# Optimization experiments

Hardware: AMD Instinct MI355X
Metric: run time of the kernel (lower is better)

Reference implementation:

```python
import jax, jax.numpy as jnp
import numpy as np
from jax import lax

NEG = -1e30  # finite stand-in for -inf so logaddexp grads stay finite


def setup_inputs() -> dict:
    key = jax.random.key(0)
    k1, k2, k3, k4, k5 = jax.random.split(key, 5)
    B, T, L, S = 16, 2048, 256, 8
    return {
        "emissions": jax.random.normal(k1, (B, T, S), dtype=jnp.float32),
        "transition": jax.random.normal(k2, (S, S), dtype=jnp.float32),
        "bos": jax.random.normal(k3, (S,), dtype=jnp.float32),
        "eos": jax.random.normal(k4, (S,), dtype=jnp.float32),
        "lengths": jnp.full((B,), T, dtype=jnp.int32),
        "targets": jax.random.randint(k5, (B, L), 0, 4, dtype=jnp.int32),
        "target_lengths": jnp.full((B,), L, dtype=jnp.int32),
    }


def _den_logz(em, lengths, transition, bos, eos):
    # Exact log-semiring forward over the fully-connected 8-state denominator CRF graph
    # (the limit of k2.intersect_dense_pruned(...).get_tot_scores(log_semiring=True)).
    B, T, S = em.shape
    alpha0 = bos[None, :] + em[:, 0, :]  # (B,S)

    def step(alpha, em_t):
        a = jax.nn.logsumexp(alpha[:, :, None] + transition[None, :, :], axis=1) + em_t
        return a, a

    _, alphas = lax.scan(step, alpha0, jnp.swapaxes(em, 0, 1)[1:])  # (T-1,B,S)
    alphas = jnp.concatenate([alpha0[None], alphas], axis=0)  # (T,B,S)
    fin = alphas[lengths - 1, jnp.arange(B)]  # (B,S) alpha at last valid frame
    return jax.nn.logsumexp(fin + eos[None, :], axis=-1)


def _num_logz(em, lengths, targets, target_lengths, transition, bos, eos):
    # Forward over the target-constrained enter/extend lattice: symbol u must be
    # entered (state targets[u]) exactly once, optionally extended (state targets[u]+4),
    # then the path moves monotonically to symbol u+1.
    B, T, S = em.shape
    L = targets.shape[1]
    b_idx = jnp.arange(B)
    es = targets          # enter-state ids, (B,L)
    xs = targets + 4      # extend-state ids, (B,L)

    t_xx = transition[xs, xs]  # extend_u -> extend_u
    t_ex = transition[es, xs]  # enter_u  -> extend_u
    prev_e = jnp.concatenate([es[:, :1], es[:, :-1]], axis=1)
    prev_x = jnp.concatenate([xs[:, :1], xs[:, :-1]], axis=1)
    t_ee = transition[prev_e, es]  # enter_{u-1}  -> enter_u
    t_xe = transition[prev_x, es]  # extend_{u-1} -> enter_u

    a_e0 = jnp.full((B, L), NEG, dtype=em.dtype)
    a_e0 = a_e0.at[:, 0].set(bos[es[:, 0]] + em[b_idx, 0, es[:, 0]])
    a_x0 = jnp.full((B, L), NEG, dtype=em.dtype)

    def shift(a):  # a[:, u-1], NEG at u=0
        return jnp.concatenate([jnp.full((B, 1), NEG, dtype=a.dtype), a[:, :-1]], axis=1)

    def step(carry, em_t):
        a_e, a_x = carry
        em_e = jnp.take_along_axis(em_t, es, axis=1)  # (B,L)
        em_x = jnp.take_along_axis(em_t, xs, axis=1)
        new_e = em_e + jnp.logaddexp(shift(a_e) + t_ee, shift(a_x) + t_xe)
        new_x = em_x + jnp.logaddexp(a_e + t_ex, a_x + t_xx)
        return (new_e, new_x), (new_e, new_x)

    _, (ae, ax) = lax.scan(step, (a_e0, a_x0), jnp.swapaxes(em, 0, 1)[1:])
    ae = jnp.concatenate([a_e0[None], ae], axis=0)  # (T,B,L)
    ax = jnp.concatenate([a_x0[None], ax], axis=0)
    fin_e = ae[lengths - 1, b_idx]  # (B,L)
    fin_x = ax[lengths - 1, b_idx]
    u = target_lengths - 1
    fe = fin_e[b_idx, u] + eos[es[b_idx, u]]
    fx = fin_x[b_idx, u] + eos[xs[b_idx, u]]
    return jnp.logaddexp(fe, fx)  # (B,)


def reference(emissions, transition, bos, eos, lengths, targets, target_lengths):
    em = emissions.astype(jnp.float32)
    logz_den = _den_logz(em, lengths, transition, bos, eos)
    logz_num = _num_logz(em, lengths, targets, target_lengths, transition, bos, eos)
    # all samples valid by construction (lengths > 0, 0 < target_len <= length)
    return jnp.mean(logz_den - logz_num)
```

## Files before the change

kernel.cpp:

```cpp
#include <hip/hip_runtime.h>
#include <math.h>


#define LOG2E 1.4426950408889634f
#define LN2   0.69314718055994531f
#define CTL_WSHL1  0x130
#define CTL_WSHR1  0x138
#define CTL_ROR(r) (0x120 + (r))

template <int CTRL>
__device__ __forceinline__ float fdpp(float x) {
    return __int_as_float(__builtin_amdgcn_update_dpp(
        0, __float_as_int(x), CTRL, 0xF, 0xF, true));
}
template <int CTRL>
__device__ __forceinline__ int idpp(int x) {
    return __builtin_amdgcn_update_dpp(0, x, CTRL, 0xF, 0xF, true);
}
__device__ __forceinline__ void cfence() { asm volatile("" ::: "memory"); }

__device__ __forceinline__ float fexp2(float x) {
#if __has_builtin(__builtin_amdgcn_exp2f)
    return __builtin_amdgcn_exp2f(x);
#else
    return exp2f(x);
#endif
}
__device__ __forceinline__ float flog2(float x) {
#if __has_builtin(__builtin_amdgcn_logf)
    return __builtin_amdgcn_logf(x);
#else
    return __log2f(x);
#endif
}
__device__ __forceinline__ float lse2(float a, float b) {
    float m = fmaxf(a, b);
    float d = fminf(a, b) - m;
    return m + flog2(1.0f + fexp2(d));
}

struct NumC { float tee[4], txe[4], tex[4], txx[4]; };

__device__ __forceinline__ void numf_step(const float2* p, float* E, float* X,
                                          float teeF, float txeF, const NumC& c) {
    float nbE = fdpp<CTL_WSHR1>(E[3]);
    float nbX = fdpp<CTL_WSHR1>(X[3]);
    float nE0 = p[0].x * fmaf(nbE,  teeF,     nbX  * txeF);
    float nE1 = p[1].x * fmaf(E[0], c.tee[1], X[0] * c.txe[1]);
    float nE2 = p[2].x * fmaf(E[1], c.tee[2], X[1] * c.txe[2]);
    float nE3 = p[3].x * fmaf(E[2], c.tee[3], X[2] * c.txe[3]);
    float nX0 = p[0].y * fmaf(E[0], c.tex[0], X[0] * c.txx[0]);
    float nX1 = p[1].y * fmaf(E[1], c.tex[1], X[1] * c.txx[1]);
    float nX2 = p[2].y * fmaf(E[2], c.tex[2], X[2] * c.txx[2]);
    float nX3 = p[3].y * fmaf(E[3], c.tex[3], X[3] * c.txx[3]);
    E[0] = nE0; E[1] = nE1; E[2] = nE2; E[3] = nE3;
    X[0] = nX0; X[1] = nX1; X[2] = nX2; X[3] = nX3;
}

__device__ __forceinline__ void numf_boundary(float* E, float* X, int& s,
                                              float& teeF, float& txeF,
                                              int lane, const NumC& c) {
    float m = fmaxf(fmaxf(fmaxf(E[0], E[1]), fmaxf(E[2], E[3])),
                    fmaxf(fmaxf(X[0], X[1]), fmaxf(X[2], X[3])));
    const bool live = (m > 0.0f);
    const int ex = live ? ((int)(__float_as_uint(m) >> 23) - 126) : 0;
    s += ex;
    const int bs = idpp<CTL_WSHR1>(s);
    if (!live) s = bs;
    int d = (lane == 0) ? 0 : (bs - s);
    const int extra = (d > 30) ? d : 0;
    s += extra; d -= extra;
    const float fsc = ldexpf(1.0f, -(ex + extra));
#pragma unroll
    for (int k = 0; k < 4; ++k) { E[k] *= fsc; X[k] *= fsc; }
    const float fs0 = (lane == 0) ? 0.0f : ldexpf(1.0f, d);
    teeF = c.tee[0] * fs0;
    txeF = c.txe[0] * fs0;
}

__device__ __forceinline__ void numb_step(const float2* p, float* bE, float* bX,
                                          const float* tex, const float* txx,
                                          const float* teeN, const float* txeN,
                                          float teeN3F, float txeN3F) {
    float mm0 = p[0].x * bE[0];
    float mm1 = p[1].x * bE[1];
    float mm2 = p[2].x * bE[2];
    float mm3 = p[3].x * bE[3];
    float m10 = p[0].y * bX[0];
    float m11 = p[1].y * bX[1];
    float m12 = p[2].y * bX[2];
    float m13 = p[3].y * bX[3];
    float mup = fdpp<CTL_WSHL1>(mm0);
    float nE0 = fmaf(tex[0], m10, teeN[0] * mm1);
    float nE1 = fmaf(tex[1], m11, teeN[1] * mm2);
    float nE2 = fmaf(tex[2], m12, teeN[2] * mm3);
    float nE3 = fmaf(tex[3], m13, teeN3F   * mup);
    float nX0 = fmaf(txx[0], m10, txeN[0] * mm1);
    float nX1 = fmaf(txx[1], m11, txeN[1] * mm2);
    float nX2 = fmaf(txx[2], m12, txeN[2] * mm3);
    float nX3 = fmaf(txx[3], m13, txeN3F   * mup);
    bE[0] = nE0; bE[1] = nE1; bE[2] = nE2; bE[3] = nE3;
    bX[0] = nX0; bX[1] = nX1; bX[2] = nX2; bX[3] = nX3;
}

__device__ __forceinline__ void numb_boundary(float* bE, float* bX, int& s,
                                              float& teeN3F, float& txeN3F,
                                              int lane, float teeN3, float txeN3) {
    float m = fmaxf(fmaxf(fmaxf(bE[0], bE[1]), fmaxf(bE[2], bE[3])),
                    fmaxf(fmaxf(bX[0], bX[1]), fmaxf(bX[2], bX[3])));
    const bool live = (m > 0.0f);
    const int ex = live ? ((int)(__float_as_uint(m) >> 23) - 126) : 0;
    s += ex;
    const int bs = idpp<CTL_WSHL1>(s);
    if (!live) s = bs;
    int d = (lane == 63) ? 0 : (bs - s);
    const int extra = (d > 30) ? d : 0;
    s += extra; d -= extra;
    const float fsc = ldexpf(1.0f, -(ex + extra));
#pragma unroll
    for (int k = 0; k < 4; ++k) { bE[k] *= fsc; bX[k] *= fsc; }
    const float fs = (lane == 63) ? 0.0f : ldexpf(1.0f, d);
    teeN3F = teeN3 * fs;
    txeN3F = txeN3 * fs;
}

__device__ __forceinline__ float denf_step(float al, float emt, const float* Tr) {
    float v1 = fdpp<CTL_ROR(1)>(al);
    float v2 = fdpp<CTL_ROR(2)>(al);
    float v3 = fdpp<CTL_ROR(3)>(al);
    float v4 = fdpp<CTL_ROR(4)>(al);
    float v5 = fdpp<CTL_ROR(5)>(al);
    float v6 = fdpp<CTL_ROR(6)>(al);
    float v7 = fdpp<CTL_ROR(7)>(al);
    float q0 = fmaf(v1, Tr[1], al * Tr[0]);
    float q1 = fmaf(v3, Tr[3], v2 * Tr[2]);
    float q2 = fmaf(v5, Tr[5], v4 * Tr[4]);
    float q3 = fmaf(v7, Tr[7], v6 * Tr[6]);
    return ((q0 + q1) + (q2 + q3)) * emt;
}
__device__ __forceinline__ float denb_step(float al, float emt, const float* TrB) {
    float g  = al * emt;
    float v1 = fdpp<CTL_ROR(7)>(g);
    float v2 = fdpp<CTL_ROR(6)>(g);
    float v3 = fdpp<CTL_ROR(5)>(g);
    float v4 = fdpp<CTL_ROR(4)>(g);
    float v5 = fdpp<CTL_ROR(3)>(g);
    float v6 = fdpp<CTL_ROR(2)>(g);
    float v7 = fdpp<CTL_ROR(1)>(g);
    float q0 = fmaf(v1, TrB[1], g * TrB[0]);
    float q1 = fmaf(v3, TrB[3], v2 * TrB[2]);
    float q2 = fmaf(v5, TrB[5], v4 * TrB[4]);
    float q3 = fmaf(v7, TrB[7], v6 * TrB[6]);
    return (q0 + q1) + (q2 + q3);
}

extern "C" __global__ void __launch_bounds__(256)
crf_fused(const float* __restrict__ em, const float* __restrict__ trans,
          const float* __restrict__ bos, const float* __restrict__ eos,
          const int* __restrict__ lengths, const int* __restrict__ targets,
          const int* __restrict__ tlens,
          float* __restrict__ ws, float* __restrict__ out,
          int B, int T, int S, int L)
{
    extern __shared__ float sm[];
    const int b    = blockIdx.x;
    const int tid  = threadIdx.x;
    const int half = S >> 1;
    const float* gem = em + (size_t)b * T * S;
    const int len = lengths[b];
    const int tm  = (len - 1) >> 1;

    float* numF  = sm + T * 8;
    float* numB  = numF + 512;
    int*   numFs = (int*)(numB + 512);
    int*   numBs = numFs + 64;
    float* denF  = (float*)(numBs + 64);
    float* denB  = denF + 8;
    int*   denFs = (int*)(denB + 8);
    int*   denBs = denFs + 8;

    for (int t = tid; t < T; t += 256) {
        const float4* gr = (const float4*)(gem + t * S);
        float4 a = gr[0], c4 = gr[1];
        float4 w0, w1;
        w0.x = fexp2(a.x * LOG2E); w0.y = fexp2(c4.x * LOG2E);
        w0.z = fexp2(a.y * LOG2E); w0.w = fexp2(c4.y * LOG2E);
        w1.x = fexp2(a.z * LOG2E); w1.y = fexp2(c4.z * LOG2E);
        w1.z = fexp2(a.w * LOG2E); w1.w = fexp2(c4.w * LOG2E);
        ((float4*)sm)[t * 2]     = w0;
        ((float4*)sm)[t * 2 + 1] = w1;
    }
    __syncthreads();

    const int wv   = tid >> 6;
    const int lane = tid & 63;
    const float2* sm2 = (const float2*)sm;

    if (wv == 0) {
        const int u0 = lane * 4;
        int e[4], ep[4];
        const int base = b * L;
#pragma unroll
        for (int k = 0; k < 4; ++k) {
            int u = u0 + k;
            e[k] = targets[base + ((u < L) ? u : (L - 1))];
        }
        ep[0] = (u0 > 0) ? targets[base + u0 - 1] : e[0];
        ep[1] = e[0]; ep[2] = e[1]; ep[3] = e[2];
        NumC c;
#pragma unroll
        for (int k = 0; k < 4; ++k) {
            c.tee[k] = fexp2(trans[ep[k] * S + e[k]] * LOG2E);
            c.txe[k] = fexp2(trans[(ep[k] + half) * S + e[k]] * LOG2E);
            c.tex[k] = fexp2(trans[e[k] * S + e[k] + half] * LOG2E);
            c.txx[k] = fexp2(trans[(e[k] + half) * S + e[k] + half] * LOG2E);
        }
        float E[4] = {0.f,0.f,0.f,0.f}, X[4] = {0.f,0.f,0.f,0.f};
        int s = 0;
        if (lane == 0) E[0] = fexp2(bos[e[0]] * LOG2E) * sm2[e[0]].x;
        float teeF = (lane == 0) ? 0.0f : c.tee[0];
        float txeF = (lane == 0) ? 0.0f : c.txe[0];

        float2 A[4][4], Bf[4][4];
        int t0 = 1;
#pragma unroll
        for (int q = 0; q < 4; ++q) {
            int tq = t0 + q; if (tq > tm) tq = (tm > 0) ? tm : 0;
#pragma unroll
            for (int k = 0; k < 4; ++k) A[q][k] = sm2[tq * 4 + e[k]];
        }
        cfence();
        while (t0 + 7 <= tm) {
#pragma unroll
            for (int q = 0; q < 4; ++q)
#pragma unroll
                for (int k = 0; k < 4; ++k)
                    Bf[q][k] = sm2[(t0 + 4 + q) * 4 + e[k]];
            cfence();
#pragma unroll
            for (int q = 0; q < 4; ++q) numf_step(A[q], E, X, teeF, txeF, c);
#pragma unroll
            for (int q = 0; q < 4; ++q) {
                int tq = t0 + 8 + q; if (tq > tm) tq = tm;
#pragma unroll
                for (int k = 0; k < 4; ++k) A[q][k] = sm2[tq * 4 + e[k]];
            }
            cfence();
#pragma unroll
            for (int q = 0; q < 4; ++q) numf_step(Bf[q], E, X, teeF, txeF, c);
            numf_boundary(E, X, s, teeF, txeF, lane, c);
            t0 += 8;
        }
        while (t0 <= tm) {
            float2 p[4];
#pragma unroll
            for (int k = 0; k < 4; ++k) p[k] = sm2[t0 * 4 + e[k]];
            numf_step(p, E, X, teeF, txeF, c);
            ++t0;
        }
#pragma unroll
        for (int k = 0; k < 4; ++k) {
            numF[lane * 8 + k]     = E[k];
            numF[lane * 8 + 4 + k] = X[k];
        }
        numFs[lane] = s;
    } else if (wv == 1) {
        const int u0 = lane * 4;
        int e[5];
        const int base = b * L;
#pragma unroll
        for (int k = 0; k < 5; ++k) {
            int u = u0 + k;
            e[k] = targets[base + ((u < L) ? u : (L - 1))];
        }
        float tex[4], txx[4], teeN[4], txeN[4];
#pragma unroll
        for (int k = 0; k < 4; ++k) {
            tex[k]  = fexp2(trans[e[k] * S + e[k] + half] * LOG2E);
            txx[k]  = fexp2(trans[(e[k] + half) * S + e[k] + half] * LOG2E);
            teeN[k] = fexp2(trans[e[k] * S + e[k + 1]] * LOG2E);
            txeN[k] = fexp2(trans[(e[k] + half) * S + e[k + 1]] * LOG2E);
        }
        if (lane == 63) { teeN[3] = 0.0f; txeN[3] = 0.0f; }
        float bE[4] = {0.f,0.f,0.f,0.f}, bX[4] = {0.f,0.f,0.f,0.f};
        const int uf = tlens[b] - 1;
        if (lane == (uf >> 2)) {
            const int kf = uf & 3;
            const int ef = e[kf];
            bE[kf] = fexp2(eos[ef] * LOG2E);
            bX[kf] = fexp2(eos[ef + half] * LOG2E);
        }
        int s = 0;
        float teeN3F = teeN[3], txeN3F = txeN[3];

        float2 A[4][4], Bf[4][4];
        int t1 = len - 1;
        const int tlo = tm + 1;
#pragma unroll
        for (int q = 0; q < 4; ++q) {
            int tq = t1 - q; if (tq < tlo) tq = tlo;
#pragma unroll
            for (int k = 0; k < 4; ++k) A[q][k] = sm2[tq * 4 + e[k]];
        }
        cfence();
        while (t1 - 7 >= tlo) {
#pragma unroll
            for (int q = 0; q < 4; ++q)
#pragma unroll
                for (int k = 0; k < 4; ++k)
                    Bf[q][k] = sm2[(t1 - 4 - q) * 4 + e[k]];
            cfence();
#pragma unroll
            for (int q = 0; q < 4; ++q)
                numb_step(A[q], bE, bX, tex, txx, teeN, txeN, teeN3F, txeN3F);
#pragma unroll
            for (int q = 0; q < 4; ++q) {
                int tq = t1 - 8 - q; if (tq < tlo) tq = tlo;
#pragma unroll
                for (int k = 0; k < 4; ++k) A[q][k] = sm2[tq * 4 + e[k]];
            }
            cfence();
#pragma unroll
            for (int q = 0; q < 4; ++q)
                numb_step(Bf[q], bE, bX, tex, txx, teeN, txeN, teeN3F, txeN3F);
            numb_boundary(bE, bX, s, teeN3F, txeN3F, lane, teeN[3], txeN[3]);
            t1 -= 8;
        }
        while (t1 >= tlo) {
            float2 p[4];
#pragma unroll
            for (int k = 0; k < 4; ++k) p[k] = sm2[t1 * 4 + e[k]];
            numb_step(p, bE, bX, tex, txx, teeN, txeN, teeN3F, txeN3F);
            --t1;
        }
#pragma unroll
        for (int k = 0; k < 4; ++k) {
            numB[lane * 8 + k]     = bE[k];
            numB[lane * 8 + 4 + k] = bX[k];
        }
        numBs[lane] = s;
    } else if (wv == 2) {
        const int j  = lane & 7;
        const int jj = ((j & 3) << 1) + (j >> 2);
        float Tr[8];
#pragma unroll
        for (int r = 0; r < 8; ++r)
            Tr[r] = fexp2(trans[((j - r) & 7) * S + j] * LOG2E);
        float al = fexp2(bos[j] * LOG2E) * sm[jj];
        int sc = 0;
        int t = 1;
        while (t + 3 <= tm) {
            float c0 = sm[t * 8 + jj];
            float c1 = sm[(t + 1) * 8 + jj];
            float c2 = sm[(t + 2) * 8 + jj];
            float c3 = sm[(t + 3) * 8 + jj];
            cfence();
            al = denf_step(al, c0, Tr);
            al = denf_step(al, c1, Tr);
            al = denf_step(al, c2, Tr);
            al = denf_step(al, c3, Tr);
            float mm = fmaxf(al, fdpp<CTL_ROR(4)>(al));
            mm = fmaxf(mm, fdpp<CTL_ROR(2)>(mm));
            mm = fmaxf(mm, fdpp<CTL_ROR(1)>(mm));
            const int ex = (int)(__float_as_uint(mm) >> 23) - 126;
            sc += ex;
            al = ldexpf(al, -ex);
            t += 4;
        }
        while (t <= tm) { al = denf_step(al, sm[t * 8 + jj], Tr); ++t; }
        if (lane < 8) { denF[j] = al; denFs[j] = sc; }
    } else {
        const int j  = lane & 7;
        const int jj = ((j & 3) << 1) + (j >> 2);
        float TrB[8];
#pragma unroll
        for (int r = 0; r < 8; ++r)
            TrB[r] = fexp2(trans[j * S + ((j + r) & 7)] * LOG2E);
        float al = fexp2(eos[j] * LOG2E);
        int sc = 0;
        int t = len - 1;
        const int tlo = tm + 1;
        while (t - 3 >= tlo) {
            float c0 = sm[t * 8 + jj];
            float c1 = sm[(t - 1) * 8 + jj];
            float c2 = sm[(t - 2) * 8 + jj];
            float c3 = sm[(t - 3) * 8 + jj];
            cfence();
            al = denb_step(al, c0, TrB);
            al = denb_step(al, c1, TrB);
            al = denb_step(al, c2, TrB);
            al = denb_step(al, c3, TrB);
            float mm = fmaxf(al, fdpp<CTL_ROR(4)>(al));
            mm = fmaxf(mm, fdpp<CTL_ROR(2)>(mm));
            mm = fmaxf(mm, fdpp<CTL_ROR(1)>(mm));
            const int ex = (int)(__float_as_uint(mm) >> 23) - 126;
            sc += ex;
            al = ldexpf(al, -ex);
            t -= 4;
        }
        while (t >= tlo) { al = denb_step(al, sm[t * 8 + jj], TrB); --t; }
        if (lane < 8) { denB[j] = al; denBs[j] = sc; }
    }

    __syncthreads();

    if (wv == 0) {
        float v = 0.0f;
#pragma unroll
        for (int k = 0; k < 8; ++k)
            v = fmaf(numF[lane * 8 + k], numB[lane * 8 + k], v);
        const int st = numFs[lane] + numBs[lane];
        float part = (v > 0.0f) ? (flog2(v) + (float)st) : -3.0e38f;
#pragma unroll
        for (int o = 1; o < 64; o <<= 1)
            part = lse2(part, __shfl_xor(part, o, 64));
        if (lane == 0) ws[b] = part;
    } else if (wv == 2) {
        if (lane < 8) {
            const float a = fmaxf(denF[lane], 1e-37f);
            const float bb = fmaxf(denB[lane], 1e-37f);
            float part = flog2(a) + flog2(bb)
                       + (float)(denFs[lane] + denBs[lane]);
            part = lse2(part, __shfl_xor(part, 1, 64));
            part = lse2(part, __shfl_xor(part, 2, 64));
            part = lse2(part, __shfl_xor(part, 4, 64));
            if (lane == 0) ws[B + b] = part;
        }
    }

    __syncthreads();
    if (tid == 0) {
        __threadfence();
        int* cnt = (int*)(ws + 2 * B);
        const int ticket = atomicAdd(cnt, 1);
        if (ticket == (int)gridDim.x - 1) {
            __threadfence();
            float acc = 0.0f;
            for (int i = 0; i < B; ++i)
                acc += atomicAdd(&ws[B + i], 0.0f) - atomicAdd(&ws[i], 0.0f);
            out[0] = acc * (LN2 / (float)B);
        }
    }
}

extern "C" void kernel_launch(void* const* d_in, const int* in_sizes, int n_in,
                              void* d_out, int out_size, void* d_ws, size_t ws_size,
                              hipStream_t stream)
{
    const float* em      = (const float*)d_in[0];
    const float* trans   = (const float*)d_in[1];
    const float* bos     = (const float*)d_in[2];
    const float* eos     = (const float*)d_in[3];
    const int*   lengths = (const int*)d_in[4];
    const int*   targets = (const int*)d_in[5];
    const int*   tlens   = (const int*)d_in[6];
    float* out = (float*)d_out;
    float* ws  = (float*)d_ws;

    const int B  = in_sizes[4];
    const int SS = in_sizes[1];
    int S = 1; while (S * S < SS) ++S;
    const int T = in_sizes[0] / (B * S);
    const int L = in_sizes[5] / B;

    const size_t shmem = (size_t)(T * 8 + 1280) * sizeof(float);

    (void)hipMemsetAsync(ws, 0, (2 * B + 1) * sizeof(float), stream);
    hipLaunchKernelGGL(crf_fused, dim3(B), dim3(256), shmem, stream,
                       em, trans, bos, eos, lengths, targets, tlens,
                       ws, out, B, T, S, L);
}
```

Measured before the change: 162.2 us.

## Split numerator forward, backward and denominator into separate blocks per sample

Launches three blocks per sample, one each for the numerator forward pass, the numerator backward pass and both denominator passes, instead of one 256-thread block doing all four. Partial results go through global workspace, and the last block to finish combines them. The numerator emission table is stored state-major so that two time steps can be fetched with one float4 LDS read. The aim is to spread the serial recurrences over more CUs and cut LDS load instructions per step, at the cost of extra global traffic and a longer final reduction on a single wave.

```diff
diff --git a/kernel.cpp b/kernel.cpp
--- a/kernel.cpp
+++ b/kernel.cpp
@@ -7,6 +7,9 @@
 #define CTL_WSHL1  0x130
 #define CTL_WSHR1  0x138
 #define CTL_ROR(r) (0x120 + (r))
+
+#define AST(p, v) __hip_atomic_store((p), (v), __ATOMIC_RELAXED, __HIP_MEMORY_SCOPE_AGENT)
+#define ALD(p)    __hip_atomic_load((p), __ATOMIC_RELAXED, __HIP_MEMORY_SCOPE_AGENT)
 
 template <int CTRL>
 __device__ __forceinline__ float fdpp(float x) {
@@ -124,6 +127,36 @@
     txeN3F = txeN3 * fs;
 }
 
+__device__ __forceinline__ void steps4_fwd(const float4 buf[4][2], float* E, float* X,
+                                           float teeF, float txeF, const NumC& c) {
+#pragma unroll
+    for (int q = 0; q < 4; ++q) {
+        float2 p[4];
+#pragma unroll
+        for (int k = 0; k < 4; ++k) {
+            const float4 v = buf[k][q >> 1];
+            p[k] = (q & 1) ? make_float2(v.z, v.w) : make_float2(v.x, v.y);
+        }
+        numf_step(p, E, X, teeF, txeF, c);
+    }
+}
+__device__ __forceinline__ void steps4_bwd(const float4 buf[4][2], float* bE, float* bX,
+                                           const float* tex, const float* txx,
+                                           const float* teeN, const float* txeN,
+                                           float teeN3F, float txeN3F) {
+#pragma unroll
+    for (int q = 0; q < 4; ++q) {
+        const int h = 1 - (q >> 1);
+        float2 p[4];
+#pragma unroll
+        for (int k = 0; k < 4; ++k) {
+            const float4 v = buf[k][h];
+            p[k] = (q & 1) ? make_float2(v.x, v.y) : make_float2(v.z, v.w);
+        }
+        numb_step(p, bE, bX, tex, txx, teeN, txeN, teeN3F, txeN3F);
+    }
+}
+
 __device__ __forceinline__ float denf_step(float al, float emt, const float* Tr) {
     float v1 = fdpp<CTL_ROR(1)>(al);
     float v2 = fdpp<CTL_ROR(2)>(al);
@@ -154,7 +187,7 @@
     return (q0 + q1) + (q2 + q3);
 }
 
-extern "C" __global__ void __launch_bounds__(256)
+extern "C" __global__ void __launch_bounds__(128)
 crf_fused(const float* __restrict__ em, const float* __restrict__ trans,
           const float* __restrict__ bos, const float* __restrict__ eos,
           const int* __restrict__ lengths, const int* __restrict__ targets,
@@ -163,40 +196,51 @@
           int B, int T, int S, int L)
 {
     extern __shared__ float sm[];
-    const int b    = blockIdx.x;
+    const int bid  = blockIdx.x;
     const int tid  = threadIdx.x;
+    const int lane = tid & 63;
+    const int wv   = tid >> 6;
     const int half = S >> 1;
+    const int role = bid / B;
+    const int b    = bid % B;
     const float* gem = em + (size_t)b * T * S;
     const int len = lengths[b];
     const int tm  = (len - 1) >> 1;
 
-    float* numF  = sm + T * 8;
-    float* numB  = numF + 512;
-    int*   numFs = (int*)(numB + 512);
-    int*   numBs = numFs + 64;
-    float* denF  = (float*)(numBs + 64);
-    float* denB  = denF + 8;
-    int*   denFs = (int*)(denB + 8);
-    int*   denBs = denFs + 8;
-
-    for (int t = tid; t < T; t += 256) {
-        const float4* gr = (const float4*)(gem + t * S);
-        float4 a = gr[0], c4 = gr[1];
-        float4 w0, w1;
-        w0.x = fexp2(a.x * LOG2E); w0.y = fexp2(c4.x * LOG2E);
-        w0.z = fexp2(a.y * LOG2E); w0.w = fexp2(c4.y * LOG2E);
-        w1.x = fexp2(a.z * LOG2E); w1.y = fexp2(c4.z * LOG2E);
-        w1.z = fexp2(a.w * LOG2E); w1.w = fexp2(c4.w * LOG2E);
-        ((float4*)sm)[t * 2]     = w0;
-        ((float4*)sm)[t * 2 + 1] = w1;
+    float* NF  = ws + 16 + (size_t)b * 576;
+    float* NB  = ws + 16 + (size_t)B * 576 + (size_t)b * 576;
+    float* DEN = ws + 16 + (size_t)(2 * B) * 576;
+    int* ticket = (int*)ws;
+
+    if (role < 2) {
+        float2* s2 = (float2*)sm;
+        for (int t = tid; t < T; t += 128) {
+            const float4* gr = (const float4*)(gem + t * S);
+            float4 a = gr[0], c4 = gr[1];
+            s2[0 * T + t] = make_float2(fexp2(a.x * LOG2E), fexp2(c4.x * LOG2E));
+            s2[1 * T + t] = make_float2(fexp2(a.y * LOG2E), fexp2(c4.y * LOG2E));
+            s2[2 * T + t] = make_float2(fexp2(a.z * LOG2E), fexp2(c4.z * LOG2E));
+            s2[3 * T + t] = make_float2(fexp2(a.w * LOG2E), fexp2(c4.w * LOG2E));
+        }
+    } else {
+        for (int t = tid; t < T; t += 128) {
+            const float4* gr = (const float4*)(gem + t * S);
+            float4 a = gr[0], c4 = gr[1];
+            float4 w0, w1;
+            w0.x = fexp2(a.x * LOG2E); w0.y = fexp2(c4.x * LOG2E);
+            w0.z = fexp2(a.y * LOG2E); w0.w = fexp2(c4.y * LOG2E);
+            w1.x = fexp2(a.z * LOG2E); w1.y = fexp2(c4.z * LOG2E);
+            w1.z = fexp2(a.w * LOG2E); w1.w = fexp2(c4.w * LOG2E);
+            ((float4*)sm)[t * 2]     = w0;
+            ((float4*)sm)[t * 2 + 1] = w1;
+        }
     }
     __syncthreads();
 
-    const int wv   = tid >> 6;
-    const int lane = tid & 63;
-    const float2* sm2 = (const float2*)sm;
-
-    if (wv == 0) {
+    if (role == 0 && wv == 0) {
+        const float2* s2 = (const float2*)sm;
+        const float4* s4 = (const float4*)sm;
+        const int Th = T >> 1;
         const int u0 = lane * 4;
         int e[4], ep[4];
         const int base = b * L;
@@ -217,54 +261,62 @@
         }
         float E[4] = {0.f,0.f,0.f,0.f}, X[4] = {0.f,0.f,0.f,0.f};
         int s = 0;
-        if (lane == 0) E[0] = fexp2(bos[e[0]] * LOG2E) * sm2[e[0]].x;
+        if (lane == 0) E[0] = fexp2(bos[e[0]] * LOG2E) * s2[e[0] * T].x;
         float teeF = (lane == 0) ? 0.0f : c.tee[0];
         float txeF = (lane == 0) ? 0.0f : c.txe[0];
 
-        float2 A[4][4], Bf[4][4];
         int t0 = 1;
-#pragma unroll
-        for (int q = 0; q < 4; ++q) {
-            int tq = t0 + q; if (tq > tm) tq = (tm > 0) ? tm : 0;
-#pragma unroll
-            for (int k = 0; k < 4; ++k) A[q][k] = sm2[tq * 4 + e[k]];
-        }
-        cfence();
-        while (t0 + 7 <= tm) {
-#pragma unroll
-            for (int q = 0; q < 4; ++q)
-#pragma unroll
-                for (int k = 0; k < 4; ++k)
-                    Bf[q][k] = sm2[(t0 + 4 + q) * 4 + e[k]];
-            cfence();
-#pragma unroll
-            for (int q = 0; q < 4; ++q) numf_step(A[q], E, X, teeF, txeF, c);
-#pragma unroll
-            for (int q = 0; q < 4; ++q) {
-                int tq = t0 + 8 + q; if (tq > tm) tq = tm;
-#pragma unroll
-                for (int k = 0; k < 4; ++k) A[q][k] = sm2[tq * 4 + e[k]];
+        while (t0 <= tm && (t0 & 1)) {
+            float2 p[4];
+#pragma unroll
+            for (int k = 0; k < 4; ++k) p[k] = s2[e[k] * T + t0];
+            numf_step(p, E, X, teeF, txeF, c);
+            ++t0;
+        }
+        float4 A[4][2], Bf[4][2];
+        if (t0 + 7 <= tm) {
+#pragma unroll
+            for (int k = 0; k < 4; ++k) {
+                A[k][0] = s4[e[k] * Th + (t0 >> 1)];
+                A[k][1] = s4[e[k] * Th + ((t0 + 2) >> 1)];
             }
             cfence();
-#pragma unroll
-            for (int q = 0; q < 4; ++q) numf_step(Bf[q], E, X, teeF, txeF, c);
-            numf_boundary(E, X, s, teeF, txeF, lane, c);
-            t0 += 8;
+            while (t0 + 7 <= tm) {
+#pragma unroll
+                for (int k = 0; k < 4; ++k) {
+                    Bf[k][0] = s4[e[k] * Th + ((t0 + 4) >> 1)];
+                    Bf[k][1] = s4[e[k] * Th + ((t0 + 6) >> 1)];
+                }
+                cfence();
+                steps4_fwd(A, E, X, teeF, txeF, c);
+#pragma unroll
+                for (int k = 0; k < 4; ++k) {
+                    A[k][0] = s4[e[k] * Th + ((t0 + 8) >> 1)];
+                    A[k][1] = s4[e[k] * Th + ((t0 + 10) >> 1)];
+                }
+                cfence();
+                steps4_fwd(Bf, E, X, teeF, txeF, c);
+                numf_boundary(E, X, s, teeF, txeF, lane, c);
+                t0 += 8;
+            }
         }
         while (t0 <= tm) {
             float2 p[4];
 #pragma unroll
-            for (int k = 0; k < 4; ++k) p[k] = sm2[t0 * 4 + e[k]];
+            for (int k = 0; k < 4; ++k) p[k] = s2[e[k] * T + t0];
             numf_step(p, E, X, teeF, txeF, c);
             ++t0;
         }
 #pragma unroll
         for (int k = 0; k < 4; ++k) {
-            numF[lane * 8 + k]     = E[k];
-            numF[lane * 8 + 4 + k] = X[k];
-        }
-        numFs[lane] = s;
-    } else if (wv == 1) {
+            AST(&NF[lane * 8 + k],     E[k]);
+            AST(&NF[lane * 8 + 4 + k], X[k]);
+        }
+        AST(&NF[512 + lane], __int_as_float(s));
+    } else if (role == 1 && wv == 0) {
+        const float2* s2 = (const float2*)sm;
+        const float4* s4 = (const float4*)sm;
+        const int Th = T >> 1;
         const int u0 = lane * 4;
         int e[5];
         const int base = b * L;
@@ -286,160 +338,166 @@
         const int uf = tlens[b] - 1;
         if (lane == (uf >> 2)) {
             const int kf = uf & 3;
-            const int ef = e[kf];
-            bE[kf] = fexp2(eos[ef] * LOG2E);
-            bX[kf] = fexp2(eos[ef + half] * LOG2E);
+            bE[kf] = fexp2(eos[e[kf]] * LOG2E);
+            bX[kf] = fexp2(eos[e[kf] + half] * LOG2E);
         }
         int s = 0;
         float teeN3F = teeN[3], txeN3F = txeN[3];
 
-        float2 A[4][4], Bf[4][4];
         int t1 = len - 1;
         const int tlo = tm + 1;
-#pragma unroll
-        for (int q = 0; q < 4; ++q) {
-            int tq = t1 - q; if (tq < tlo) tq = tlo;
-#pragma unroll
-            for (int k = 0; k < 4; ++k) A[q][k] = sm2[tq * 4 + e[k]];
-        }
-        cfence();
-        while (t1 - 7 >= tlo) {
-#pragma unroll
-            for (int q = 0; q < 4; ++q)
-#pragma unroll
-                for (int k = 0; k < 4; ++k)
-                    Bf[q][k] = sm2[(t1 - 4 - q) * 4 + e[k]];
-            cfence();
-#pragma unroll
-            for (int q = 0; q < 4; ++q)
-                numb_step(A[q], bE, bX, tex, txx, teeN, txeN, teeN3F, txeN3F);
-#pragma unroll
-            for (int q = 0; q < 4; ++q) {
-                int tq = t1 - 8 - q; if (tq < tlo) tq = tlo;
-#pragma unroll
-                for (int k = 0; k < 4; ++k) A[q][k] = sm2[tq * 4 + e[k]];
+        while (t1 >= tlo && !(t1 & 1)) {
+            float2 p[4];
+#pragma unroll
+            for (int k = 0; k < 4; ++k) p[k] = s2[e[k] * T + t1];
+            numb_step(p, bE, bX, tex, txx, teeN, txeN, teeN3F, txeN3F);
+            --t1;
+        }
+        float4 A[4][2], Bf[4][2];
+        if (t1 - 7 >= tlo) {
+#pragma unroll
+            for (int k = 0; k < 4; ++k) {
+                A[k][0] = s4[e[k] * Th + ((t1 - 3) >> 1)];
+                A[k][1] = s4[e[k] * Th + ((t1 - 1) >> 1)];
             }
             cfence();
-#pragma unroll
-            for (int q = 0; q < 4; ++q)
-                numb_step(Bf[q], bE, bX, tex, txx, teeN, txeN, teeN3F, txeN3F);
-            numb_boundary(bE, bX, s, teeN3F, txeN3F, lane, teeN[3], txeN[3]);
-            t1 -= 8;
+            while (t1 - 7 >= tlo) {
+#pragma unroll
+                for (int k = 0; k < 4; ++k) {
+                    Bf[k][0] = s4[e[k] * Th + ((t1 - 7) >> 1)];
+                    Bf[k][1] = s4[e[k] * Th + ((t1 - 5) >> 1)];
+                }
+                cfence();
+                steps4_bwd(A, bE, bX, tex, txx, teeN, txeN, teeN3F, txeN3F);
+                const int ta = (t1 - 11 > 0) ? (t1 - 11) : 0;
+#pragma unroll
+                for (int k = 0; k < 4; ++k) {
+                    A[k][0] = s4[e[k] * Th + (ta >> 1)];
+                    A[k][1] = s4[e[k] * Th + ((ta + 2) >> 1)];
+                }
+                cfence();
+                steps4_bwd(Bf, bE, bX, tex, txx, teeN, txeN, teeN3F, txeN3F);
+                numb_boundary(bE, bX, s, teeN3F, txeN3F, lane, teeN[3], txeN[3]);
+                t1 -= 8;
+            }
         }
         while (t1 >= tlo) {
             float2 p[4];
 #pragma unroll
-            for (int k = 0; k < 4; ++k) p[k] = sm2[t1 * 4 + e[k]];
+            for (int k = 0; k < 4; ++k) p[k] = s2[e[k] * T + t1];
             numb_step(p, bE, bX, tex, txx, teeN, txeN, teeN3F, txeN3F);
             --t1;
         }
 #pragma unroll
         for (int k = 0; k < 4; ++k) {
-            numB[lane * 8 + k]     = bE[k];
-            numB[lane * 8 + 4 + k] = bX[k];
-        }
-        numBs[lane] = s;
-    } else if (wv == 2) {
+            AST(&NB[lane * 8 + k],     bE[k]);
+            AST(&NB[lane * 8 + 4 + k], bX[k]);
+        }
+        AST(&NB[512 + lane], __int_as_float(s));
+    } else if (role == 2) {
+        float* denF  = sm + T * 8;
+        float* denB  = denF + 8;
+        int*   denFs = (int*)(denB + 8);
+        int*   denBs = denFs + 8;
         const int j  = lane & 7;
         const int jj = ((j & 3) << 1) + (j >> 2);
-        float Tr[8];
-#pragma unroll
-        for (int r = 0; r < 8; ++r)
-            Tr[r] = fexp2(trans[((j - r) & 7) * S + j] * LOG2E);
-        float al = fexp2(bos[j] * LOG2E) * sm[jj];
-        int sc = 0;
-        int t = 1;
-        while (t + 3 <= tm) {
-            float c0 = sm[t * 8 + jj];
-            float c1 = sm[(t + 1) * 8 + jj];
-            float c2 = sm[(t + 2) * 8 + jj];
-            float c3 = sm[(t + 3) * 8 + jj];
-            cfence();
-            al = denf_step(al, c0, Tr);
-            al = denf_step(al, c1, Tr);
-            al = denf_step(al, c2, Tr);
-            al = denf_step(al, c3, Tr);
-            float mm = fmaxf(al, fdpp<CTL_ROR(4)>(al));
-            mm = fmaxf(mm, fdpp<CTL_ROR(2)>(mm));
-            mm = fmaxf(mm, fdpp<CTL_ROR(1)>(mm));
-            const int ex = (int)(__float_as_uint(mm) >> 23) - 126;
-            sc += ex;
-            al = ldexpf(al, -ex);
-            t += 4;
-        }
-        while (t <= tm) { al = denf_step(al, sm[t * 8 + jj], Tr); ++t; }
-        if (lane < 8) { denF[j] = al; denFs[j] = sc; }
-    } else {
-        const int j  = lane & 7;
-        const int jj = ((j & 3) << 1) + (j >> 2);
-        float TrB[8];
-#pragma unroll
-        for (int r = 0; r < 8; ++r)
-            TrB[r] = fexp2(trans[j * S + ((j + r) & 7)] * LOG2E);
-        float al = fexp2(eos[j] * LOG2E);
-        int sc = 0;
-        int t = len - 1;
-        const int tlo = tm + 1;
-        while (t - 3 >= tlo) {
-            float c0 = sm[t * 8 + jj];
-            float c1 = sm[(t - 1) * 8 + jj];
-            float c2 = sm[(t - 2) * 8 + jj];
-            float c3 = sm[(t - 3) * 8 + jj];
-            cfence();
-            al = denb_step(al, c0, TrB);
-            al = denb_step(al, c1, TrB);
-            al = denb_step(al, c2, TrB);
-            al = denb_step(al, c3, TrB);
-            float mm = fmaxf(al, fdpp<CTL_ROR(4)>(al));
-            mm = fmaxf(mm, fdpp<CTL_ROR(2)>(mm));
-            mm = fmaxf(mm, fdpp<CTL_ROR(1)>(mm));
-            const int ex = (int)(__float_as_uint(mm) >> 23) - 126;
-            sc += ex;
-            al = ldexpf(al, -ex);
-            t -= 4;
-        }
-        while (t >= tlo) { al = denb_step(al, sm[t * 8 + jj], TrB); --t; }
-        if (lane < 8) { denB[j] = al; denBs[j] = sc; }
-    }
-
-    __syncthreads();
-
-    if (wv == 0) {
-        float v = 0.0f;
-#pragma unroll
-        for (int k = 0; k < 8; ++k)
-            v = fmaf(numF[lane * 8 + k], numB[lane * 8 + k], v);
-        const int st = numFs[lane] + numBs[lane];
-        float part = (v > 0.0f) ? (flog2(v) + (float)st) : -3.0e38f;
-#pragma unroll
-        for (int o = 1; o < 64; o <<= 1)
-            part = lse2(part, __shfl_xor(part, o, 64));
-        if (lane == 0) ws[b] = part;
-    } else if (wv == 2) {
-        if (lane < 8) {
-            const float a = fmaxf(denF[lane], 1e-37f);
-            const float bb = fmaxf(denB[lane], 1e-37f);
-            float part = flog2(a) + flog2(bb)
-                       + (float)(denFs[lane] + denBs[lane]);
+        if (wv == 0) {
+            float Tr[8];
+#pragma unroll
+            for (int r = 0; r < 8; ++r)
+                Tr[r] = fexp2(trans[((j - r) & 7) * S + j] * LOG2E);
+            float al = fexp2(bos[j] * LOG2E) * sm[jj];
+            int sc = 0;
+            int t = 1;
+            while (t + 3 <= tm) {
+                float c0 = sm[t * 8 + jj];
+                float c1 = sm[(t + 1) * 8 + jj];
+                float c2 = sm[(t + 2) * 8 + jj];
+                float c3 = sm[(t + 3) * 8 + jj];
+                cfence();
+                al = denf_step(al, c0, Tr);
+                al = denf_step(al, c1, Tr);
+                al = denf_step(al, c2, Tr);
+                al = denf_step(al, c3, Tr);
+                float mm = fmaxf(al, fdpp<CTL_ROR(4)>(al));
+                mm = fmaxf(mm, fdpp<CTL_ROR(2)>(mm));
+                mm = fmaxf(mm, fdpp<CTL_ROR(1)>(mm));
+                const int ex = (int)(__float_as_uint(mm) >> 23) - 126;
+                sc += ex;
+                al = ldexpf(al, -ex);
+                t += 4;
+            }
+            while (t <= tm) { al = denf_step(al, sm[t * 8 + jj], Tr); ++t; }
+            if (lane < 8) { denF[j] = al; denFs[j] = sc; }
+        } else {
+            float TrB[8];
+#pragma unroll
+            for (int r = 0; r < 8; ++r)
+                TrB[r] = fexp2(trans[j * S + ((j + r) & 7)] * LOG2E);
+            float al = fexp2(eos[j] * LOG2E);
+            int sc = 0;
+            int t = len - 1;
+            const int tlo = tm + 1;
+            while (t - 3 >= tlo) {
+                float c0 = sm[t * 8 + jj];
+                float c1 = sm[(t - 1) * 8 + jj];
+                float c2 = sm[(t - 2) * 8 + jj];
+                float c3 = sm[(t - 3) * 8 + jj];
+                cfence();
+                al = denb_step(al, c0, TrB);
+                al = denb_step(al, c1, TrB);
+                al = denb_step(al, c2, TrB);
+                al = denb_step(al, c3, TrB);
+                float mm = fmaxf(al, fdpp<CTL_ROR(4)>(al));
+                mm = fmaxf(mm, fdpp<CTL_ROR(2)>(mm));
+                mm = fmaxf(mm, fdpp<CTL_ROR(1)>(mm));
+                const int ex = (int)(__float_as_uint(mm) >> 23) - 126;
+                sc += ex;
+                al = ldexpf(al, -ex);
+                t -= 4;
+            }
+            while (t >= tlo) { al = denb_step(al, sm[t * 8 + jj], TrB); --t; }
+            if (lane < 8) { denB[j] = al; denBs[j] = sc; }
+        }
+        __syncthreads();
+        if (wv == 0 && lane < 8) {
+            const float a  = fmaxf(denF[j], 1e-37f);
+            const float bb = fmaxf(denB[j], 1e-37f);
+            float part = flog2(a) + flog2(bb) + (float)(denFs[j] + denBs[j]);
             part = lse2(part, __shfl_xor(part, 1, 64));
             part = lse2(part, __shfl_xor(part, 2, 64));
             part = lse2(part, __shfl_xor(part, 4, 64));
-            if (lane == 0) ws[B + b] = part;
+            if (j == 0) AST(&DEN[b], part);
         }
     }
 
     __syncthreads();
+    int* wflag = (int*)sm;
     if (tid == 0) {
         __threadfence();
-        int* cnt = (int*)(ws + 2 * B);
-        const int ticket = atomicAdd(cnt, 1);
-        if (ticket == (int)gridDim.x - 1) {
-            __threadfence();
-            float acc = 0.0f;
-            for (int i = 0; i < B; ++i)
-                acc += atomicAdd(&ws[B + i], 0.0f) - atomicAdd(&ws[i], 0.0f);
-            out[0] = acc * (LN2 / (float)B);
-        }
+        const int tk = atomicAdd(ticket, 1);
+        wflag[0] = (tk == 3 * B - 1) ? 1 : 0;
+    }
+    __syncthreads();
+    if (wflag[0] && tid < 64) {
+        __threadfence();
+        float acc = 0.0f;
+        for (int bb2 = 0; bb2 < B; ++bb2) {
+            const float* nf = ws + 16 + (size_t)bb2 * 576;
+            const float* nb = ws + 16 + (size_t)B * 576 + (size_t)bb2 * 576;
+            float v = 0.0f;
+#pragma unroll
+            for (int k = 0; k < 8; ++k)
+                v = fmaf(ALD(&nf[lane * 8 + k]), ALD(&nb[lane * 8 + k]), v);
+            const int st = __float_as_int(ALD(&nf[512 + lane]))
+                         + __float_as_int(ALD(&nb[512 + lane]));
+            float part = (v > 0.0f) ? (flog2(v) + (float)st) : -3.0e38f;
+#pragma unroll
+            for (int o = 1; o < 64; o <<= 1)
+                part = lse2(part, __shfl_xor(part, o, 64));
+            if (lane == 0) acc += ALD(&DEN[bb2]) - part;
+        }
+        if (lane == 0) out[0] = acc * (LN2 / (float)B);
     }
 }
 
@@ -463,10 +521,10 @@
     const int T = in_sizes[0] / (B * S);
     const int L = in_sizes[5] / B;
 
-    const size_t shmem = (size_t)(T * 8 + 1280) * sizeof(float);
-
-    (void)hipMemsetAsync(ws, 0, (2 * B + 1) * sizeof(float), stream);
-    hipLaunchKernelGGL(crf_fused, dim3(B), dim3(256), shmem, stream,
+    const size_t shmem = (size_t)(T * 8 + 64) * sizeof(float);
+
+    (void)hipMemsetAsync(ws, 0, 64, stream);
+    hipLaunchKernelGGL(crf_fused, dim3(3 * B), dim3(128), shmem, stream,
                        em, trans, bos, eos, lengths, targets, tlens,
                        ws, out, B, T, S, L);
 }
```

Measured after the change: 162.7 us. About the same (+0.3%).
